# Performance work log

Hardware: AMD Instinct MI355X
Metric: run time of the kernel (lower is better)

Reference implementation:

```python
import jax, jax.numpy as jnp
import numpy as np

N, F, E = 1024, 32, 20


def setup_inputs() -> dict:
    key = jax.random.key(0)
    ks = jax.random.split(key, 18)
    f32 = jnp.float32
    nrm = lambda k, shape, s=1.0: (jax.random.normal(k, shape, f32) * s)
    scalar = nrm(ks[0], (N, 1, F))
    vector = nrm(ks[1], (N, 3, F))
    expansion = nrm(ks[2], (N, N, E))
    d = nrm(ks[3], (N, N, 3))
    direction = d / (jnp.linalg.norm(d, axis=-1, keepdims=True) + 1e-6)
    mask = (jax.random.uniform(ks[4], (N, N, 1)) < 0.9).astype(f32)
    w = 0.1  # weight scale
    return {
        "scalar": scalar, "vector": vector, "expansion": expansion,
        "direction": direction, "mask": mask,
        # message.msg_left: Linear(F,F) -> SiLU -> Linear(F,3F)
        "mL_w1": nrm(ks[5], (F, F), w), "mL_b1": jnp.zeros((F,), f32),
        "mL_w2": nrm(ks[6], (F, 3 * F), w), "mL_b2": jnp.zeros((3 * F,), f32),
        # message.msg_right: Linear(E, 3F)
        "mR_w": nrm(ks[7], (E, 3 * F), w), "mR_b": jnp.zeros((3 * F,), f32),
        # update.upd_right: Linear(2F,F) -> SiLU -> Linear(F,3F)
        "uR_w1": nrm(ks[8], (2 * F, F), w), "uR_b1": jnp.zeros((F,), f32),
        "uR_w2": nrm(ks[9], (F, 3 * F), w), "uR_b2": jnp.zeros((3 * F,), f32),
        # update.U / update.V: Linear(F,F,bias=False)
        "U_w": nrm(ks[10], (F, F), w),
        "V_w": nrm(ks[11], (F, F), w),
    }


def _message(s, v, expansion, direction, mask,
             mL_w1, mL_b1, mL_w2, mL_b2, mR_w, mR_b):
    # msg_left(s): [N,1,F] -> [N,1,3F]
    left = jax.nn.silu(s @ mL_w1 + mL_b1) @ mL_w2 + mL_b2
    # msg_right(expansion): [N,N,E] -> [N,N,3F] -> [N,N,1,3F]
    right = (expansion @ mR_w + mR_b)[..., None, :]
    prod = left * right                      # [N,N,1,3F]
    a, b, c = jnp.split(prod, 3, axis=-1)    # each [N,N,1,F]
    mask_ = mask[..., None]                  # [N,N,1,1]
    delta_s = jnp.sum(mask_ * b, axis=-3)    # [N,1,F]
    dv = v * a + direction[..., None] * c    # [N,N,3,F]
    delta_v = jnp.sum(mask_ * dv, axis=-3)   # [N,3,F]
    return delta_s, delta_v


def _update(scalar, vector, uR_w1, uR_b1, uR_w2, uR_b2, U_w, V_w):
    left = vector @ U_w                      # [N,3,F]
    right = vector @ V_w                     # [N,3,F]
    right_norm = jnp.linalg.norm(right, axis=-2, keepdims=True)   # [N,1,F]
    feats = jnp.concatenate((scalar, right_norm), axis=-1)        # [N,1,2F]
    feats = jax.nn.silu(feats @ uR_w1 + uR_b1) @ uR_w2 + uR_b2    # [N,1,3F]
    a, b, c = jnp.split(feats, 3, axis=-1)
    delta_v = a * left                                            # [N,3,F]
    inner = jnp.sum(left * right, axis=-2, keepdims=True)         # [N,1,F]
    delta_s = inner * b + c
    return delta_s, delta_v


def reference(scalar, vector, expansion, direction, mask,
              mL_w1, mL_b1, mL_w2, mL_b2, mR_w, mR_b,
              uR_w1, uR_b1, uR_w2, uR_b2, U_w, V_w):
    ds, dv = _message(scalar, vector, expansion, direction, mask,
                      mL_w1, mL_b1, mL_w2, mL_b2, mR_w, mR_b)
    scalar = scalar + ds
    vector = vector + dv
    ds, dv = _update(scalar, vector, uR_w1, uR_b1, uR_w2, uR_b2, U_w, V_w)
    return scalar + ds, vector + dv
```

## Files before the change

### kernel.cpp

```cpp
#include <hip/hip_runtime.h>
#include <hip/hip_bf16.h>
#include <math.h>

#define NN 1024
#define KJ 32
#define NCHUNK (NN / KJ)
#define LP 40

typedef __attribute__((ext_vector_type(8))) short v8s;
typedef __attribute__((ext_vector_type(4))) float v4f;

#define MFMA(a, b, c) __builtin_amdgcn_mfma_f32_16x16x32_bf16((a), (b), (c), 0, 0, 0)

static __device__ __forceinline__ float silu_f(float x) {
    return x / (1.0f + __expf(-x));
}
static __device__ __forceinline__ unsigned short f2bf(float x) {
    __hip_bfloat16 h = __float2bfloat16(x);
    unsigned short u; __builtin_memcpy(&u, &h, 2); return u;
}
static __device__ __forceinline__ unsigned pack2bf(float lo, float hi) {
    __hip_bfloat162 h = __float22bfloat162_rn(make_float2(lo, hi));
    unsigned u; __builtin_memcpy(&u, &h, 4); return u;
}

extern "C" __global__ __launch_bounds__(128)
void node_kernel(const float* __restrict__ scalar,
                 const float* __restrict__ vector,
                 const float* __restrict__ mL_w1, const float* __restrict__ mL_b1,
                 const float* __restrict__ mL_w2, const float* __restrict__ mL_b2,
                 unsigned short* __restrict__ RT)
{
    const int j = blockIdx.x;
    const int t = threadIdx.x;
    __shared__ float ss[32], sh[32], sleft[96];

    if (t < 32) ss[t] = scalar[j * 32 + t];
    __syncthreads();
    if (t < 32) {
        float a = mL_b1[t];
        #pragma unroll
        for (int k = 0; k < 32; k++) a = fmaf(ss[k], mL_w1[k * 32 + t], a);
        sh[t] = silu_f(a);
    }
    __syncthreads();
    if (t < 96) {
        float a = mL_b2[t];
        #pragma unroll
        for (int k = 0; k < 32; k++) a = fmaf(sh[k], mL_w2[k * 96 + t], a);
        sleft[t] = a;
    }
    __syncthreads();
    for (int n = t; n < 160; n += 128) {
        float val;
        if (n < 32)        val = sleft[32 + n];
        else if (n < 128)  val = vector[j * 96 + (n - 32)] * sleft[(n - 32) & 31];
        else               val = sleft[64 + (n - 128)];
        RT[(size_t)n * NN + j] = f2bf(val);
    }
}

extern "C" __global__ __launch_bounds__(128, 3)
void edge_mfma_kernel(const float* __restrict__ scalar,
                      const float* __restrict__ vector,
                      const float* __restrict__ expansion,
                      const float* __restrict__ direction,
                      const float* __restrict__ mask,
                      const float* __restrict__ mR_w, const float* __restrict__ mR_b,
                      const float* __restrict__ uR_w1, const float* __restrict__ uR_b1,
                      const float* __restrict__ uR_w2, const float* __restrict__ uR_b2,
                      const float* __restrict__ U_w,  const float* __restrict__ V_w,
                      const unsigned short* __restrict__ RT,
                      float* __restrict__ out)
{
    const int i = blockIdx.x;
    const int t = threadIdx.x;
    const int wave = t >> 6;
    const int lane = t & 63;
    const int lrow = lane & 15;
    const int quad = lane >> 4;
    const int jp = lane >> 2;
    const int g  = lane & 3;
    const int jl = jp * 2;

    __shared__ __align__(16) char smem[18944];
    unsigned short* L1 = (unsigned short*)smem;
    unsigned short* L2 = (unsigned short*)(smem + 2560);
    float* T1c = (float*)smem;
    float* T2c = (float*)(smem + 10752);
    __shared__ float snew[32], vnew[96], lUs[96], rVs[96], rnorm[32], h2s[32], f2s[96];

    v4f acc[16];
    #pragma unroll
    for (int q = 0; q < 16; ++q) acc[q] = (v4f){0.f, 0.f, 0.f, 0.f};

    if (wave == 0) {
        for (int ch = 0; ch < NCHUNK; ++ch) {
            const int j0 = ch * KJ;
            const size_t jg = (size_t)i * NN + j0 + jl;
            const float4 fa = *(const float4*)(expansion + jg * 20 + 4 * g);
            const float4 fb = *(const float4*)(expansion + (jg + 1) * 20 + 4 * g);
            const float m0 = mask[jg], m1 = mask[jg + 1];
            {
                const float ea[4] = {fa.x, fa.y, fa.z, fa.w};
                const float eb[4] = {fb.x, fb.y, fb.z, fb.w};
                #pragma unroll
                for (int k = 0; k < 4; ++k)
                    *(unsigned*)(L1 + (4 * g + k) * LP + jl) = pack2bf(m0 * ea[k], m1 * eb[k]);
            }
            if (g == 3) {
                const float4 ca = *(const float4*)(expansion + jg * 20 + 16);
                const float4 cb = *(const float4*)(expansion + (jg + 1) * 20 + 16);
                const float ea[4] = {ca.x, ca.y, ca.z, ca.w};
                const float eb[4] = {cb.x, cb.y, cb.z, cb.w};
                #pragma unroll
                for (int k = 0; k < 4; ++k)
                    *(unsigned*)(L1 + (16 + k) * LP + jl) = pack2bf(m0 * ea[k], m1 * eb[k]);
            }
            if (g == 0) *(unsigned*)(L1 + 20 * LP + jl) = pack2bf(m0, m1);

            const int koff = quad * 8;
            const v8s a0 = *(const v8s*)(L1 + lrow * LP + koff);
            const v8s a1 = *(const v8s*)(L1 + (16 + lrow) * LP + koff);
            const unsigned short* Bp = RT + (size_t)lrow * NN + j0 + koff;
            #pragma unroll
            for (int nt = 0; nt < 8; ++nt) {
                const v8s b = *(const v8s*)(Bp + (size_t)nt * 16 * NN);
                acc[nt]     = MFMA(a0, b, acc[nt]);
                acc[8 + nt] = MFMA(a1, b, acc[8 + nt]);
            }
        }
    } else {
        for (int ch = 0; ch < NCHUNK; ++ch) {
            const int j0 = ch * KJ;
            const size_t jg = (size_t)i * NN + j0 + jl;
            const float m0 = mask[jg], m1 = mask[jg + 1];
            const float pa[3] = {m0 * direction[jg * 3 + 0],
                                 m0 * direction[jg * 3 + 1],
                                 m0 * direction[jg * 3 + 2]};
            const float pb[3] = {m1 * direction[(jg + 1) * 3 + 0],
                                 m1 * direction[(jg + 1) * 3 + 1],
                                 m1 * direction[(jg + 1) * 3 + 2]};
            const float4 fa = *(const float4*)(expansion + jg * 20 + 4 * g);
            const float4 fb = *(const float4*)(expansion + (jg + 1) * 20 + 4 * g);
            const float ea[4] = {fa.x, fa.y, fa.z, fa.w};
            const float eb[4] = {fb.x, fb.y, fb.z, fb.w};
            #pragma unroll
            for (int d = 0; d < 3; ++d)
                #pragma unroll
                for (int k = 0; k < 4; ++k)
                    *(unsigned*)(L2 + (d * 20 + 4 * g + k) * LP + jl) =
                        pack2bf(pa[d] * ea[k], pb[d] * eb[k]);
            if (g < 3) {
                const float4 ca = *(const float4*)(expansion + jg * 20 + 16);
                const float4 cb = *(const float4*)(expansion + (jg + 1) * 20 + 16);
                const float sa = (g == 0) ? pa[0] : ((g == 1) ? pa[1] : pa[2]);
                const float sb = (g == 0) ? pb[0] : ((g == 1) ? pb[1] : pb[2]);
                const float ea4[4] = {ca.x, ca.y, ca.z, ca.w};
                const float eb4[4] = {cb.x, cb.y, cb.z, cb.w};
                #pragma unroll
                for (int k = 0; k < 4; ++k)
                    *(unsigned*)(L2 + (g * 20 + 16 + k) * LP + jl) =
                        pack2bf(sa * ea4[k], sb * eb4[k]);
            } else {
                #pragma unroll
                for (int d = 0; d < 3; ++d)
                    *(unsigned*)(L2 + (60 + d) * LP + jl) = pack2bf(pa[d], pb[d]);
            }

            const int koff = quad * 8;
            const v8s c0 = *(const v8s*)(L2 + (lrow) * LP + koff);
            const v8s c1 = *(const v8s*)(L2 + (16 + lrow) * LP + koff);
            const v8s c2 = *(const v8s*)(L2 + (32 + lrow) * LP + koff);
            const v8s c3 = *(const v8s*)(L2 + (48 + lrow) * LP + koff);
            const unsigned short* Bp = RT + (size_t)(128 + lrow) * NN + j0 + koff;
            const v8s b0 = *(const v8s*)(Bp);
            const v8s b1 = *(const v8s*)(Bp + (size_t)16 * NN);
            acc[0] = MFMA(c0, b0, acc[0]); acc[1] = MFMA(c0, b1, acc[1]);
            acc[2] = MFMA(c1, b0, acc[2]); acc[3] = MFMA(c1, b1, acc[3]);
            acc[4] = MFMA(c2, b0, acc[4]); acc[5] = MFMA(c2, b1, acc[5]);
            acc[6] = MFMA(c3, b0, acc[6]); acc[7] = MFMA(c3, b1, acc[7]);
        }
    }

    __syncthreads();
    if (wave == 0) {
        #pragma unroll
        for (int mt = 0; mt < 2; ++mt)
        #pragma unroll
        for (int nt = 0; nt < 8; ++nt)
        #pragma unroll
        for (int r = 0; r < 4; ++r) {
            const int row = mt * 16 + quad * 4 + r;
            if (row <= 20) T1c[row * 128 + nt * 16 + lrow] = acc[mt * 8 + nt][r];
        }
    } else {
        #pragma unroll
        for (int mt = 0; mt < 4; ++mt)
        #pragma unroll
        for (int nb = 0; nb < 2; ++nb)
        #pragma unroll
        for (int r = 0; r < 4; ++r) {
            const int row = mt * 16 + quad * 4 + r;
            if (row <= 62) T2c[row * 32 + nb * 16 + lrow] = acc[mt * 2 + nb][r];
        }
    }
    __syncthreads();

    if (t < 32) {
        const int f = t;
        float a = mR_b[32 + f] * T1c[20 * 128 + f];
        #pragma unroll
        for (int e = 0; e < 20; ++e) a = fmaf(mR_w[e * 96 + 32 + f], T1c[e * 128 + f], a);
        snew[f] = scalar[i * 32 + f] + a;
    } else if (t < 128) {
        const int q = t - 32, d = q >> 5, f = q & 31;
        const int col = 32 + q;
        float a = mR_b[f] * T1c[20 * 128 + col];
        #pragma unroll
        for (int e = 0; e < 20; ++e) a = fmaf(mR_w[e * 96 + f], T1c[e * 128 + col], a);
        float c = mR_b[64 + f] * T2c[(60 + d) * 32 + f];
        #pragma unroll
        for (int e = 0; e < 20; ++e) c = fmaf(mR_w[e * 96 + 64 + f], T2c[(d * 20 + e) * 32 + f], c);
        vnew[q] = vector[i * 96 + q] + a + c;
    }
    __syncthreads();

    if (t < 96) {
        const int d = t >> 5, f = t & 31;
        float au = 0.f, av = 0.f;
        #pragma unroll
        for (int k = 0; k < 32; ++k) {
            const float vv = vnew[d * 32 + k];
            au = fmaf(vv, U_w[k * 32 + f], au);
            av = fmaf(vv, V_w[k * 32 + f], av);
        }
        lUs[t] = au; rVs[t] = av;
    }
    __syncthreads();
    if (t < 32)
        rnorm[t] = sqrtf(rVs[t] * rVs[t] + rVs[32 + t] * rVs[32 + t] + rVs[64 + t] * rVs[64 + t]);
    __syncthreads();
    if (t < 32) {
        float a = uR_b1[t];
        #pragma unroll
        for (int k = 0; k < 32; ++k) a = fmaf(snew[k], uR_w1[k * 32 + t], a);
        #pragma unroll
        for (int k = 0; k < 32; ++k) a = fmaf(rnorm[k], uR_w1[(32 + k) * 32 + t], a);
        h2s[t] = silu_f(a);
    }
    __syncthreads();
    if (t < 96) {
        float a = uR_b2[t];
        #pragma unroll
        for (int k = 0; k < 32; ++k) a = fmaf(h2s[k], uR_w2[k * 96 + t], a);
        f2s[t] = a;
    }
    __syncthreads();
    if (t < 32) {
        const float inner = lUs[t] * rVs[t] + lUs[32 + t] * rVs[32 + t] + lUs[64 + t] * rVs[64 + t];
        out[i * 32 + t] = snew[t] + inner * f2s[32 + t] + f2s[64 + t];
    }
    if (t < 96) {
        out[32768 + i * 96 + t] = vnew[t] + f2s[t & 31] * lUs[t];
    }
}

extern "C" void kernel_launch(void* const* d_in, const int* in_sizes, int n_in,
                              void* d_out, int out_size, void* d_ws, size_t ws_size,
                              hipStream_t stream) {
    const float* scalar    = (const float*)d_in[0];
    const float* vector    = (const float*)d_in[1];
    const float* expansion = (const float*)d_in[2];
    const float* direction = (const float*)d_in[3];
    const float* mask      = (const float*)d_in[4];
    const float* mL_w1     = (const float*)d_in[5];
    const float* mL_b1     = (const float*)d_in[6];
    const float* mL_w2     = (const float*)d_in[7];
    const float* mL_b2     = (const float*)d_in[8];
    const float* mR_w      = (const float*)d_in[9];
    const float* mR_b      = (const float*)d_in[10];
    const float* uR_w1     = (const float*)d_in[11];
    const float* uR_b1     = (const float*)d_in[12];
    const float* uR_w2     = (const float*)d_in[13];
    const float* uR_b2     = (const float*)d_in[14];
    const float* U_w       = (const float*)d_in[15];
    const float* V_w       = (const float*)d_in[16];
    float* out = (float*)d_out;
    unsigned short* RT = (unsigned short*)d_ws;

    hipLaunchKernelGGL(node_kernel, dim3(NN), dim3(128), 0, stream,
                       scalar, vector, mL_w1, mL_b1, mL_w2, mL_b2, RT);
    hipLaunchKernelGGL(edge_mfma_kernel, dim3(NN), dim3(128), 0, stream,
                       scalar, vector, expansion, direction, mask,
                       mR_w, mR_b, uR_w1, uR_b1, uR_w2, uR_b2, U_w, V_w,
                       RT, out);
}
```

Baseline: 229.8 us.

## Split edge reduction across four waves and prefetch next chunk's inputs

The edge kernel now runs 256 threads, so each of the two roles (expansion path and direction path) is handled by two waves. Each wave reduces half of the j-chunks, and the partial accumulators are summed through shared memory in an extra synchronized pass. Each wave also loads the next chunk's expansion, mask and direction values into registers before processing the current chunk, hiding global-load latency. This raises parallelism and memory-level concurrency per block, at the cost of more register pressure, an added reduction step and more LDS staging. Threads 128-255 are idle during the epilogue.

```diff
diff --git a/kernel.cpp b/kernel.cpp
--- a/kernel.cpp
+++ b/kernel.cpp
@@ -5,6 +5,7 @@
 #define NN 1024
 #define KJ 32
 #define NCHUNK (NN / KJ)
+#define HCH (NCHUNK / 2)
 #define LP 40
 
 typedef __attribute__((ext_vector_type(8))) short v8s;
@@ -60,7 +61,7 @@
     }
 }
 
-extern "C" __global__ __launch_bounds__(128, 3)
+extern "C" __global__ __launch_bounds__(256, 4)
 void edge_mfma_kernel(const float* __restrict__ scalar,
                       const float* __restrict__ vector,
                       const float* __restrict__ expansion,
@@ -82,10 +83,11 @@
     const int jp = lane >> 2;
     const int g  = lane & 3;
     const int jl = jp * 2;
+    const int half = wave & 1;
 
     __shared__ __align__(16) char smem[18944];
-    unsigned short* L1 = (unsigned short*)smem;
-    unsigned short* L2 = (unsigned short*)(smem + 2560);
+    unsigned short* L1 = (unsigned short*)smem + half * (32 * LP);
+    unsigned short* L2 = (unsigned short*)(smem + 5120) + half * (64 * LP);
     float* T1c = (float*)smem;
     float* T2c = (float*)(smem + 10752);
     __shared__ float snew[32], vnew[96], lUs[96], rVs[96], rnorm[32], h2s[32], f2s[96];
@@ -94,13 +96,34 @@
     #pragma unroll
     for (int q = 0; q < 16; ++q) acc[q] = (v4f){0.f, 0.f, 0.f, 0.f};
 
-    if (wave == 0) {
-        for (int ch = 0; ch < NCHUNK; ++ch) {
-            const int j0 = ch * KJ;
-            const size_t jg = (size_t)i * NN + j0 + jl;
-            const float4 fa = *(const float4*)(expansion + jg * 20 + 4 * g);
-            const float4 fb = *(const float4*)(expansion + (jg + 1) * 20 + 4 * g);
-            const float m0 = mask[jg], m1 = mask[jg + 1];
+    const int ch0 = half * HCH;
+    const int chEnd = ch0 + HCH;
+
+    if (wave < 2) {
+        float4 fa, fb, ca, cb; float m0, m1;
+        {
+            const size_t jg = (size_t)i * NN + ch0 * KJ + jl;
+            fa = *(const float4*)(expansion + jg * 20 + 4 * g);
+            fb = *(const float4*)(expansion + (jg + 1) * 20 + 4 * g);
+            m0 = mask[jg]; m1 = mask[jg + 1];
+            if (g == 3) {
+                ca = *(const float4*)(expansion + jg * 20 + 16);
+                cb = *(const float4*)(expansion + (jg + 1) * 20 + 16);
+            } else { ca = fa; cb = fb; }
+        }
+        for (int ch = ch0; ch < chEnd; ++ch) {
+            float4 nfa, nfb, nca, ncb; float nm0, nm1;
+            {
+                const int pch = (ch + 1 < chEnd) ? (ch + 1) : ch;
+                const size_t jg = (size_t)i * NN + pch * KJ + jl;
+                nfa = *(const float4*)(expansion + jg * 20 + 4 * g);
+                nfb = *(const float4*)(expansion + (jg + 1) * 20 + 4 * g);
+                nm0 = mask[jg]; nm1 = mask[jg + 1];
+                if (g == 3) {
+                    nca = *(const float4*)(expansion + jg * 20 + 16);
+                    ncb = *(const float4*)(expansion + (jg + 1) * 20 + 16);
+                } else { nca = nfa; ncb = nfb; }
+            }
             {
                 const float ea[4] = {fa.x, fa.y, fa.z, fa.w};
                 const float eb[4] = {fb.x, fb.y, fb.z, fb.w};
@@ -109,8 +132,6 @@
                     *(unsigned*)(L1 + (4 * g + k) * LP + jl) = pack2bf(m0 * ea[k], m1 * eb[k]);
             }
             if (g == 3) {
-                const float4 ca = *(const float4*)(expansion + jg * 20 + 16);
-                const float4 cb = *(const float4*)(expansion + (jg + 1) * 20 + 16);
                 const float ea[4] = {ca.x, ca.y, ca.z, ca.w};
                 const float eb[4] = {cb.x, cb.y, cb.z, cb.w};
                 #pragma unroll
@@ -119,6 +140,7 @@
             }
             if (g == 0) *(unsigned*)(L1 + 20 * LP + jl) = pack2bf(m0, m1);
 
+            const int j0 = ch * KJ;
             const int koff = quad * 8;
             const v8s a0 = *(const v8s*)(L1 + lrow * LP + koff);
             const v8s a1 = *(const v8s*)(L1 + (16 + lrow) * LP + koff);
@@ -129,45 +151,64 @@
                 acc[nt]     = MFMA(a0, b, acc[nt]);
                 acc[8 + nt] = MFMA(a1, b, acc[8 + nt]);
             }
+            fa = nfa; fb = nfb; ca = nca; cb = ncb; m0 = nm0; m1 = nm1;
         }
     } else {
-        for (int ch = 0; ch < NCHUNK; ++ch) {
-            const int j0 = ch * KJ;
-            const size_t jg = (size_t)i * NN + j0 + jl;
-            const float m0 = mask[jg], m1 = mask[jg + 1];
-            const float pa[3] = {m0 * direction[jg * 3 + 0],
-                                 m0 * direction[jg * 3 + 1],
-                                 m0 * direction[jg * 3 + 2]};
-            const float pb[3] = {m1 * direction[(jg + 1) * 3 + 0],
-                                 m1 * direction[(jg + 1) * 3 + 1],
-                                 m1 * direction[(jg + 1) * 3 + 2]};
-            const float4 fa = *(const float4*)(expansion + jg * 20 + 4 * g);
-            const float4 fb = *(const float4*)(expansion + (jg + 1) * 20 + 4 * g);
-            const float ea[4] = {fa.x, fa.y, fa.z, fa.w};
-            const float eb[4] = {fb.x, fb.y, fb.z, fb.w};
-            #pragma unroll
-            for (int d = 0; d < 3; ++d)
-                #pragma unroll
-                for (int k = 0; k < 4; ++k)
-                    *(unsigned*)(L2 + (d * 20 + 4 * g + k) * LP + jl) =
-                        pack2bf(pa[d] * ea[k], pb[d] * eb[k]);
+        float4 fa, fb, ca, cb; float m0, m1, da0, da1, da2, db0, db1, db2;
+        {
+            const size_t jg = (size_t)i * NN + ch0 * KJ + jl;
+            fa = *(const float4*)(expansion + jg * 20 + 4 * g);
+            fb = *(const float4*)(expansion + (jg + 1) * 20 + 4 * g);
+            m0 = mask[jg]; m1 = mask[jg + 1];
+            da0 = direction[jg * 3 + 0]; da1 = direction[jg * 3 + 1]; da2 = direction[jg * 3 + 2];
+            db0 = direction[(jg + 1) * 3 + 0]; db1 = direction[(jg + 1) * 3 + 1]; db2 = direction[(jg + 1) * 3 + 2];
             if (g < 3) {
-                const float4 ca = *(const float4*)(expansion + jg * 20 + 16);
-                const float4 cb = *(const float4*)(expansion + (jg + 1) * 20 + 16);
-                const float sa = (g == 0) ? pa[0] : ((g == 1) ? pa[1] : pa[2]);
-                const float sb = (g == 0) ? pb[0] : ((g == 1) ? pb[1] : pb[2]);
-                const float ea4[4] = {ca.x, ca.y, ca.z, ca.w};
-                const float eb4[4] = {cb.x, cb.y, cb.z, cb.w};
-                #pragma unroll
-                for (int k = 0; k < 4; ++k)
-                    *(unsigned*)(L2 + (g * 20 + 16 + k) * LP + jl) =
-                        pack2bf(sa * ea4[k], sb * eb4[k]);
-            } else {
+                ca = *(const float4*)(expansion + jg * 20 + 16);
+                cb = *(const float4*)(expansion + (jg + 1) * 20 + 16);
+            } else { ca = fa; cb = fb; }
+        }
+        for (int ch = ch0; ch < chEnd; ++ch) {
+            float4 nfa, nfb, nca, ncb; float nm0, nm1, nda0, nda1, nda2, ndb0, ndb1, ndb2;
+            {
+                const int pch = (ch + 1 < chEnd) ? (ch + 1) : ch;
+                const size_t jg = (size_t)i * NN + pch * KJ + jl;
+                nfa = *(const float4*)(expansion + jg * 20 + 4 * g);
+                nfb = *(const float4*)(expansion + (jg + 1) * 20 + 4 * g);
+                nm0 = mask[jg]; nm1 = mask[jg + 1];
+                nda0 = direction[jg * 3 + 0]; nda1 = direction[jg * 3 + 1]; nda2 = direction[jg * 3 + 2];
+                ndb0 = direction[(jg + 1) * 3 + 0]; ndb1 = direction[(jg + 1) * 3 + 1]; ndb2 = direction[(jg + 1) * 3 + 2];
+                if (g < 3) {
+                    nca = *(const float4*)(expansion + jg * 20 + 16);
+                    ncb = *(const float4*)(expansion + (jg + 1) * 20 + 16);
+                } else { nca = nfa; ncb = nfb; }
+            }
+            {
+                const float pa[3] = {m0 * da0, m0 * da1, m0 * da2};
+                const float pb[3] = {m1 * db0, m1 * db1, m1 * db2};
+                const float ea[4] = {fa.x, fa.y, fa.z, fa.w};
+                const float eb[4] = {fb.x, fb.y, fb.z, fb.w};
                 #pragma unroll
                 for (int d = 0; d < 3; ++d)
-                    *(unsigned*)(L2 + (60 + d) * LP + jl) = pack2bf(pa[d], pb[d]);
-            }
-
+                    #pragma unroll
+                    for (int k = 0; k < 4; ++k)
+                        *(unsigned*)(L2 + (d * 20 + 4 * g + k) * LP + jl) =
+                            pack2bf(pa[d] * ea[k], pb[d] * eb[k]);
+                if (g < 3) {
+                    const float sa = (g == 0) ? pa[0] : ((g == 1) ? pa[1] : pa[2]);
+                    const float sb = (g == 0) ? pb[0] : ((g == 1) ? pb[1] : pb[2]);
+                    const float ea4[4] = {ca.x, ca.y, ca.z, ca.w};
+                    const float eb4[4] = {cb.x, cb.y, cb.z, cb.w};
+                    #pragma unroll
+                    for (int k = 0; k < 4; ++k)
+                        *(unsigned*)(L2 + (g * 20 + 16 + k) * LP + jl) =
+                            pack2bf(sa * ea4[k], sb * eb4[k]);
+                } else {
+                    #pragma unroll
+                    for (int d = 0; d < 3; ++d)
+                        *(unsigned*)(L2 + (60 + d) * LP + jl) = pack2bf(pa[d], pb[d]);
+                }
+            }
+            const int j0 = ch * KJ;
             const int koff = quad * 8;
             const v8s c0 = *(const v8s*)(L2 + (lrow) * LP + koff);
             const v8s c1 = *(const v8s*)(L2 + (16 + lrow) * LP + koff);
@@ -180,6 +221,8 @@
             acc[2] = MFMA(c1, b0, acc[2]); acc[3] = MFMA(c1, b1, acc[3]);
             acc[4] = MFMA(c2, b0, acc[4]); acc[5] = MFMA(c2, b1, acc[5]);
             acc[6] = MFMA(c3, b0, acc[6]); acc[7] = MFMA(c3, b1, acc[7]);
+            fa = nfa; fb = nfb; ca = nca; cb = ncb; m0 = nm0; m1 = nm1;
+            da0 = nda0; da1 = nda1; da2 = nda2; db0 = ndb0; db1 = ndb1; db2 = ndb2;
         }
     }
 
@@ -194,7 +237,7 @@
             const int row = mt * 16 + quad * 4 + r;
             if (row <= 20) T1c[row * 128 + nt * 16 + lrow] = acc[mt * 8 + nt][r];
         }
-    } else {
+    } else if (wave == 2) {
         #pragma unroll
         for (int mt = 0; mt < 4; ++mt)
         #pragma unroll
@@ -203,6 +246,28 @@
         for (int r = 0; r < 4; ++r) {
             const int row = mt * 16 + quad * 4 + r;
             if (row <= 62) T2c[row * 32 + nb * 16 + lrow] = acc[mt * 2 + nb][r];
+        }
+    }
+    __syncthreads();
+    if (wave == 1) {
+        #pragma unroll
+        for (int mt = 0; mt < 2; ++mt)
+        #pragma unroll
+        for (int nt = 0; nt < 8; ++nt)
+        #pragma unroll
+        for (int r = 0; r < 4; ++r) {
+            const int row = mt * 16 + quad * 4 + r;
+            if (row <= 20) T1c[row * 128 + nt * 16 + lrow] += acc[mt * 8 + nt][r];
+        }
+    } else if (wave == 3) {
+        #pragma unroll
+        for (int mt = 0; mt < 4; ++mt)
+        #pragma unroll
+        for (int nb = 0; nb < 2; ++nb)
+        #pragma unroll
+        for (int r = 0; r < 4; ++r) {
+            const int row = mt * 16 + quad * 4 + r;
+            if (row <= 62) T2c[row * 32 + nb * 16 + lrow] += acc[mt * 2 + nb][r];
         }
     }
     __syncthreads();
@@ -291,7 +356,7 @@
 
     hipLaunchKernelGGL(node_kernel, dim3(NN), dim3(128), 0, stream,
                        scalar, vector, mL_w1, mL_b1, mL_w2, mL_b2, RT);
-    hipLaunchKernelGGL(edge_mfma_kernel, dim3(NN), dim3(128), 0, stream,
+    hipLaunchKernelGGL(edge_mfma_kernel, dim3(NN), dim3(256), 0, stream,
                        scalar, vector, expansion, direction, mask,
                        mR_w, mR_b, uR_w1, uR_b1, uR_w2, uR_b2, U_w, V_w,
                        RT, out);
```

Measured after the change: 216.0 us. 1.06x faster.

## Split edge reduction over j-slices with LDS-staged RT and atomic partials

Applied to the files above, without the earlier changes.

Restructures the edge kernel so each block handles 8 nodes by a 64-wide j slice. The slice of the RT matrix is staged once in LDS and reused by all four waves, each covering two i rows, instead of every block streaming RT from global memory. Expansion, mask and direction loads are prefetched one step ahead. Partial results are reduced into a zeroed workspace via atomicAdd, and the node-update tail moves to a separate combine kernel. This adds a memset, a third launch and atomic traffic in exchange for better reuse and more parallel work.

```diff
diff --git a/kernel.cpp b/kernel.cpp
--- a/kernel.cpp
+++ b/kernel.cpp
@@ -3,9 +3,10 @@
 #include <math.h>
 
 #define NN 1024
-#define KJ 32
-#define NCHUNK (NN / KJ)
+#define JS 64
+#define PB 72
 #define LP 40
+#define LROWS 85
 
 typedef __attribute__((ext_vector_type(8))) short v8s;
 typedef __attribute__((ext_vector_type(4))) float v4f;
@@ -60,20 +61,14 @@
     }
 }
 
-extern "C" __global__ __launch_bounds__(128, 3)
-void edge_mfma_kernel(const float* __restrict__ scalar,
-                      const float* __restrict__ vector,
-                      const float* __restrict__ expansion,
+extern "C" __global__ __launch_bounds__(256, 3)
+void edge_mfma_kernel(const float* __restrict__ expansion,
                       const float* __restrict__ direction,
                       const float* __restrict__ mask,
                       const float* __restrict__ mR_w, const float* __restrict__ mR_b,
-                      const float* __restrict__ uR_w1, const float* __restrict__ uR_b1,
-                      const float* __restrict__ uR_w2, const float* __restrict__ uR_b2,
-                      const float* __restrict__ U_w,  const float* __restrict__ V_w,
                       const unsigned short* __restrict__ RT,
-                      float* __restrict__ out)
+                      float* __restrict__ part)
 {
-    const int i = blockIdx.x;
     const int t = threadIdx.x;
     const int wave = t >> 6;
     const int lane = t & 63;
@@ -83,186 +78,228 @@
     const int g  = lane & 3;
     const int jl = jp * 2;
 
-    __shared__ __align__(16) char smem[18944];
-    unsigned short* L1 = (unsigned short*)smem;
-    unsigned short* L2 = (unsigned short*)(smem + 2560);
-    float* T1c = (float*)smem;
-    float* T2c = (float*)(smem + 10752);
-    __shared__ float snew[32], vnew[96], lUs[96], rVs[96], rnorm[32], h2s[32], f2s[96];
-
-    v4f acc[16];
+    const int bx = blockIdx.x;
+    const int slice = bx & 15;
+    const int i0 = (bx >> 4) * 8;
+    const int j0s = slice * JS;
+
+    __shared__ __align__(16) unsigned short BSm[160 * PB];
+    __shared__ __align__(16) unsigned short Lm[4 * LROWS * LP];
+
+    for (int u = t; u < 160 * 8; u += 256) {
+        const int row = u >> 3, seg = u & 7;
+        *(uint4*)(BSm + row * PB + seg * 8) =
+            *(const uint4*)(RT + (size_t)row * NN + j0s + seg * 8);
+    }
+    __syncthreads();
+
+    unsigned short* L1 = Lm + wave * (LROWS * LP);
+    unsigned short* L2 = L1 + 21 * LP;
+    float* S = (float*)L1;
+
+    v4f acc[24];
     #pragma unroll
-    for (int q = 0; q < 16; ++q) acc[q] = (v4f){0.f, 0.f, 0.f, 0.f};
-
-    if (wave == 0) {
-        for (int ch = 0; ch < NCHUNK; ++ch) {
-            const int j0 = ch * KJ;
-            const size_t jg = (size_t)i * NN + j0 + jl;
-            const float4 fa = *(const float4*)(expansion + jg * 20 + 4 * g);
-            const float4 fb = *(const float4*)(expansion + (jg + 1) * 20 + 4 * g);
-            const float m0 = mask[jg], m1 = mask[jg + 1];
+    for (int q = 0; q < 24; ++q) acc[q] = (v4f){0.f, 0.f, 0.f, 0.f};
+
+    const int iw = i0 + wave * 2;
+
+    float4 fa, fb, ca, cb;
+    float m0, m1, da0, da1, da2, db0, db1, db2;
+    {
+        const size_t jg = (size_t)iw * NN + j0s + jl;
+        fa = *(const float4*)(expansion + jg * 20 + 4 * g);
+        fb = *(const float4*)(expansion + (jg + 1) * 20 + 4 * g);
+        ca = *(const float4*)(expansion + jg * 20 + 16);
+        cb = *(const float4*)(expansion + (jg + 1) * 20 + 16);
+        m0 = mask[jg]; m1 = mask[jg + 1];
+        da0 = direction[jg * 3 + 0]; da1 = direction[jg * 3 + 1]; da2 = direction[jg * 3 + 2];
+        db0 = direction[(jg + 1) * 3 + 0]; db1 = direction[(jg + 1) * 3 + 1]; db2 = direction[(jg + 1) * 3 + 2];
+    }
+
+    for (int it = 0; it < 2; ++it) {
+        const int i = iw + it;
+        for (int ch = 0; ch < 2; ++ch) {
             {
+                const float pa0 = m0 * da0, pa1 = m0 * da1, pa2 = m0 * da2;
+                const float pb0 = m1 * db0, pb1 = m1 * db1, pb2 = m1 * db2;
                 const float ea[4] = {fa.x, fa.y, fa.z, fa.w};
                 const float eb[4] = {fb.x, fb.y, fb.z, fb.w};
+                const float caa[4] = {ca.x, ca.y, ca.z, ca.w};
+                const float cbb[4] = {cb.x, cb.y, cb.z, cb.w};
                 #pragma unroll
                 for (int k = 0; k < 4; ++k)
                     *(unsigned*)(L1 + (4 * g + k) * LP + jl) = pack2bf(m0 * ea[k], m1 * eb[k]);
-            }
-            if (g == 3) {
-                const float4 ca = *(const float4*)(expansion + jg * 20 + 16);
-                const float4 cb = *(const float4*)(expansion + (jg + 1) * 20 + 16);
-                const float ea[4] = {ca.x, ca.y, ca.z, ca.w};
-                const float eb[4] = {cb.x, cb.y, cb.z, cb.w};
-                #pragma unroll
-                for (int k = 0; k < 4; ++k)
-                    *(unsigned*)(L1 + (16 + k) * LP + jl) = pack2bf(m0 * ea[k], m1 * eb[k]);
-            }
-            if (g == 0) *(unsigned*)(L1 + 20 * LP + jl) = pack2bf(m0, m1);
-
-            const int koff = quad * 8;
-            const v8s a0 = *(const v8s*)(L1 + lrow * LP + koff);
-            const v8s a1 = *(const v8s*)(L1 + (16 + lrow) * LP + koff);
-            const unsigned short* Bp = RT + (size_t)lrow * NN + j0 + koff;
-            #pragma unroll
-            for (int nt = 0; nt < 8; ++nt) {
-                const v8s b = *(const v8s*)(Bp + (size_t)nt * 16 * NN);
-                acc[nt]     = MFMA(a0, b, acc[nt]);
-                acc[8 + nt] = MFMA(a1, b, acc[8 + nt]);
-            }
-        }
-    } else {
-        for (int ch = 0; ch < NCHUNK; ++ch) {
-            const int j0 = ch * KJ;
-            const size_t jg = (size_t)i * NN + j0 + jl;
-            const float m0 = mask[jg], m1 = mask[jg + 1];
-            const float pa[3] = {m0 * direction[jg * 3 + 0],
-                                 m0 * direction[jg * 3 + 1],
-                                 m0 * direction[jg * 3 + 2]};
-            const float pb[3] = {m1 * direction[(jg + 1) * 3 + 0],
-                                 m1 * direction[(jg + 1) * 3 + 1],
-                                 m1 * direction[(jg + 1) * 3 + 2]};
-            const float4 fa = *(const float4*)(expansion + jg * 20 + 4 * g);
-            const float4 fb = *(const float4*)(expansion + (jg + 1) * 20 + 4 * g);
-            const float ea[4] = {fa.x, fa.y, fa.z, fa.w};
-            const float eb[4] = {fb.x, fb.y, fb.z, fb.w};
-            #pragma unroll
-            for (int d = 0; d < 3; ++d)
-                #pragma unroll
-                for (int k = 0; k < 4; ++k)
-                    *(unsigned*)(L2 + (d * 20 + 4 * g + k) * LP + jl) =
-                        pack2bf(pa[d] * ea[k], pb[d] * eb[k]);
-            if (g < 3) {
-                const float4 ca = *(const float4*)(expansion + jg * 20 + 16);
-                const float4 cb = *(const float4*)(expansion + (jg + 1) * 20 + 16);
-                const float sa = (g == 0) ? pa[0] : ((g == 1) ? pa[1] : pa[2]);
-                const float sb = (g == 0) ? pb[0] : ((g == 1) ? pb[1] : pb[2]);
-                const float ea4[4] = {ca.x, ca.y, ca.z, ca.w};
-                const float eb4[4] = {cb.x, cb.y, cb.z, cb.w};
-                #pragma unroll
-                for (int k = 0; k < 4; ++k)
-                    *(unsigned*)(L2 + (g * 20 + 16 + k) * LP + jl) =
-                        pack2bf(sa * ea4[k], sb * eb4[k]);
-            } else {
+                if (g == 3) {
+                    #pragma unroll
+                    for (int k = 0; k < 4; ++k)
+                        *(unsigned*)(L1 + (16 + k) * LP + jl) = pack2bf(m0 * caa[k], m1 * cbb[k]);
+                }
+                if (g == 0) *(unsigned*)(L1 + 20 * LP + jl) = pack2bf(m0, m1);
+
+                const float pad[3] = {pa0, pa1, pa2};
+                const float pbd[3] = {pb0, pb1, pb2};
                 #pragma unroll
                 for (int d = 0; d < 3; ++d)
-                    *(unsigned*)(L2 + (60 + d) * LP + jl) = pack2bf(pa[d], pb[d]);
-            }
-
-            const int koff = quad * 8;
-            const v8s c0 = *(const v8s*)(L2 + (lrow) * LP + koff);
-            const v8s c1 = *(const v8s*)(L2 + (16 + lrow) * LP + koff);
-            const v8s c2 = *(const v8s*)(L2 + (32 + lrow) * LP + koff);
-            const v8s c3 = *(const v8s*)(L2 + (48 + lrow) * LP + koff);
-            const unsigned short* Bp = RT + (size_t)(128 + lrow) * NN + j0 + koff;
-            const v8s b0 = *(const v8s*)(Bp);
-            const v8s b1 = *(const v8s*)(Bp + (size_t)16 * NN);
-            acc[0] = MFMA(c0, b0, acc[0]); acc[1] = MFMA(c0, b1, acc[1]);
-            acc[2] = MFMA(c1, b0, acc[2]); acc[3] = MFMA(c1, b1, acc[3]);
-            acc[4] = MFMA(c2, b0, acc[4]); acc[5] = MFMA(c2, b1, acc[5]);
-            acc[6] = MFMA(c3, b0, acc[6]); acc[7] = MFMA(c3, b1, acc[7]);
+                    #pragma unroll
+                    for (int k = 0; k < 4; ++k)
+                        *(unsigned*)(L2 + (d * 20 + 4 * g + k) * LP + jl) =
+                            pack2bf(pad[d] * ea[k], pbd[d] * eb[k]);
+                if (g < 3) {
+                    const float sa = (g == 0) ? pa0 : ((g == 1) ? pa1 : pa2);
+                    const float sb = (g == 0) ? pb0 : ((g == 1) ? pb1 : pb2);
+                    #pragma unroll
+                    for (int k = 0; k < 4; ++k)
+                        *(unsigned*)(L2 + (g * 20 + 16 + k) * LP + jl) =
+                            pack2bf(sa * caa[k], sb * cbb[k]);
+                } else {
+                    *(unsigned*)(L2 + (60 + 0) * LP + jl) = pack2bf(pa0, pb0);
+                    *(unsigned*)(L2 + (60 + 1) * LP + jl) = pack2bf(pa1, pb1);
+                    *(unsigned*)(L2 + (60 + 2) * LP + jl) = pack2bf(pa2, pb2);
+                }
+            }
+            {
+                const int u = it * 2 + ch;
+                const int un = (u < 3) ? u + 1 : 3;
+                const int itn = un >> 1, chn = un & 1;
+                const size_t jg = (size_t)(iw + itn) * NN + j0s + chn * 32 + jl;
+                fa = *(const float4*)(expansion + jg * 20 + 4 * g);
+                fb = *(const float4*)(expansion + (jg + 1) * 20 + 4 * g);
+                ca = *(const float4*)(expansion + jg * 20 + 16);
+                cb = *(const float4*)(expansion + (jg + 1) * 20 + 16);
+                m0 = mask[jg]; m1 = mask[jg + 1];
+                da0 = direction[jg * 3 + 0]; da1 = direction[jg * 3 + 1]; da2 = direction[jg * 3 + 2];
+                db0 = direction[(jg + 1) * 3 + 0]; db1 = direction[(jg + 1) * 3 + 1]; db2 = direction[(jg + 1) * 3 + 2];
+            }
+            {
+                const int ko = quad * 8;
+                const int kl = ch * 32 + ko;
+                const v8s a0 = *(const v8s*)(L1 + lrow * LP + ko);
+                const v8s a1 = *(const v8s*)(L1 + (16 + lrow) * LP + ko);
+                #pragma unroll
+                for (int nt = 0; nt < 8; ++nt) {
+                    const v8s b = *(const v8s*)(BSm + (nt * 16 + lrow) * PB + kl);
+                    acc[nt]     = MFMA(a0, b, acc[nt]);
+                    acc[8 + nt] = MFMA(a1, b, acc[8 + nt]);
+                }
+                const v8s c0 = *(const v8s*)(L2 + (lrow) * LP + ko);
+                const v8s c1 = *(const v8s*)(L2 + (16 + lrow) * LP + ko);
+                const v8s c2 = *(const v8s*)(L2 + (32 + lrow) * LP + ko);
+                const v8s c3 = *(const v8s*)(L2 + (48 + lrow) * LP + ko);
+                const v8s b0 = *(const v8s*)(BSm + (128 + lrow) * PB + kl);
+                const v8s b1 = *(const v8s*)(BSm + (144 + lrow) * PB + kl);
+                acc[16] = MFMA(c0, b0, acc[16]); acc[17] = MFMA(c0, b1, acc[17]);
+                acc[18] = MFMA(c1, b0, acc[18]); acc[19] = MFMA(c1, b1, acc[19]);
+                acc[20] = MFMA(c2, b0, acc[20]); acc[21] = MFMA(c2, b1, acc[21]);
+                acc[22] = MFMA(c3, b0, acc[22]); acc[23] = MFMA(c3, b1, acc[23]);
+            }
         }
-    }
-
-    __syncthreads();
-    if (wave == 0) {
-        #pragma unroll
-        for (int mt = 0; mt < 2; ++mt)
-        #pragma unroll
-        for (int nt = 0; nt < 8; ++nt)
-        #pragma unroll
-        for (int r = 0; r < 4; ++r) {
-            const int row = mt * 16 + quad * 4 + r;
-            if (row <= 20) T1c[row * 128 + nt * 16 + lrow] = acc[mt * 8 + nt][r];
+
+        #pragma unroll
+        for (int h = 0; h < 2; ++h) {
+            #pragma unroll
+            for (int mt = 0; mt < 2; ++mt)
+            #pragma unroll
+            for (int q = 0; q < 4; ++q)
+            #pragma unroll
+            for (int r = 0; r < 4; ++r) {
+                const int row = mt * 16 + quad * 4 + r;
+                if (row <= 20) S[row * 64 + q * 16 + lrow] = acc[mt * 8 + h * 4 + q][r];
+            }
+            const int col = h * 64 + lane;
+            const int fw = (col < 32) ? (32 + col) : ((col - 32) & 31);
+            float v = mR_b[fw] * S[20 * 64 + lane];
+            #pragma unroll
+            for (int e = 0; e < 20; ++e) v = fmaf(mR_w[e * 96 + fw], S[e * 64 + lane], v);
+            atomicAdd(part + (size_t)i * 224 + col, v);
         }
-    } else {
-        #pragma unroll
-        for (int mt = 0; mt < 4; ++mt)
-        #pragma unroll
-        for (int nb = 0; nb < 2; ++nb)
-        #pragma unroll
-        for (int r = 0; r < 4; ++r) {
-            const int row = mt * 16 + quad * 4 + r;
-            if (row <= 62) T2c[row * 32 + nb * 16 + lrow] = acc[mt * 2 + nb][r];
+        #pragma unroll
+        for (int h2 = 0; h2 < 2; ++h2) {
+            #pragma unroll
+            for (int mt = 0; mt < 4; ++mt)
+            #pragma unroll
+            for (int r = 0; r < 4; ++r) {
+                const int row = mt * 16 + quad * 4 + r;
+                if (row <= 62) S[row * 16 + lrow] = acc[16 + mt * 2 + h2][r];
+            }
+            if (lane < 48) {
+                const int dd = lane >> 4, f16 = lane & 15;
+                const int f = h2 * 16 + f16;
+                float v = mR_b[64 + f] * S[(60 + dd) * 16 + f16];
+                #pragma unroll
+                for (int e = 0; e < 20; ++e)
+                    v = fmaf(mR_w[e * 96 + 64 + f], S[(dd * 20 + e) * 16 + f16], v);
+                atomicAdd(part + (size_t)i * 224 + 128 + dd * 32 + f, v);
+            }
         }
-    }
-    __syncthreads();
-
+        #pragma unroll
+        for (int q = 0; q < 24; ++q) acc[q] = (v4f){0.f, 0.f, 0.f, 0.f};
+    }
+}
+
+extern "C" __global__ __launch_bounds__(256)
+void combine_kernel(const float* __restrict__ scalar,
+                    const float* __restrict__ vector,
+                    const float* __restrict__ uR_w1, const float* __restrict__ uR_b1,
+                    const float* __restrict__ uR_w2, const float* __restrict__ uR_b2,
+                    const float* __restrict__ U_w,  const float* __restrict__ V_w,
+                    const float* __restrict__ part,
+                    float* __restrict__ out)
+{
+    const int i = blockIdx.x;
+    const int t = threadIdx.x;
+    __shared__ float snew[32], vnew[96];
+    __shared__ float lU[96], rV[96], rnorm[32], h2[32], f2[96];
+
+    if (t < 128) {
+        float a = part[(size_t)i * 224 + t];
+        if (t >= 32) a += part[(size_t)i * 224 + 96 + t];
+        const int d = t >> 5, ff = t & 31;
+        if (d == 0) snew[ff] = scalar[i * 32 + ff] + a;
+        else        vnew[(d - 1) * 32 + ff] = vector[i * 96 + (d - 1) * 32 + ff] + a;
+    }
+    __syncthreads();
+
+    if (t < 96) {
+        const int d = t >> 5, ff = t & 31;
+        float a = 0.0f;
+        #pragma unroll
+        for (int k = 0; k < 32; k++) a = fmaf(vnew[d * 32 + k], U_w[k * 32 + ff], a);
+        lU[t] = a;
+    } else if (t >= 128 && t < 224) {
+        const int dt = t - 128, d = dt >> 5, ff = dt & 31;
+        float a = 0.0f;
+        #pragma unroll
+        for (int k = 0; k < 32; k++) a = fmaf(vnew[d * 32 + k], V_w[k * 32 + ff], a);
+        rV[dt] = a;
+    }
+    __syncthreads();
     if (t < 32) {
-        const int f = t;
-        float a = mR_b[32 + f] * T1c[20 * 128 + f];
-        #pragma unroll
-        for (int e = 0; e < 20; ++e) a = fmaf(mR_w[e * 96 + 32 + f], T1c[e * 128 + f], a);
-        snew[f] = scalar[i * 32 + f] + a;
-    } else if (t < 128) {
-        const int q = t - 32, d = q >> 5, f = q & 31;
-        const int col = 32 + q;
-        float a = mR_b[f] * T1c[20 * 128 + col];
-        #pragma unroll
-        for (int e = 0; e < 20; ++e) a = fmaf(mR_w[e * 96 + f], T1c[e * 128 + col], a);
-        float c = mR_b[64 + f] * T2c[(60 + d) * 32 + f];
-        #pragma unroll
-        for (int e = 0; e < 20; ++e) c = fmaf(mR_w[e * 96 + 64 + f], T2c[(d * 20 + e) * 32 + f], c);
-        vnew[q] = vector[i * 96 + q] + a + c;
-    }
-    __syncthreads();
-
-    if (t < 96) {
-        const int d = t >> 5, f = t & 31;
-        float au = 0.f, av = 0.f;
-        #pragma unroll
-        for (int k = 0; k < 32; ++k) {
-            const float vv = vnew[d * 32 + k];
-            au = fmaf(vv, U_w[k * 32 + f], au);
-            av = fmaf(vv, V_w[k * 32 + f], av);
-        }
-        lUs[t] = au; rVs[t] = av;
-    }
-    __syncthreads();
-    if (t < 32)
-        rnorm[t] = sqrtf(rVs[t] * rVs[t] + rVs[32 + t] * rVs[32 + t] + rVs[64 + t] * rVs[64 + t]);
+        const float a = rV[t] * rV[t] + rV[32 + t] * rV[32 + t] + rV[64 + t] * rV[64 + t];
+        rnorm[t] = sqrtf(a);
+    }
     __syncthreads();
     if (t < 32) {
         float a = uR_b1[t];
         #pragma unroll
-        for (int k = 0; k < 32; ++k) a = fmaf(snew[k], uR_w1[k * 32 + t], a);
-        #pragma unroll
-        for (int k = 0; k < 32; ++k) a = fmaf(rnorm[k], uR_w1[(32 + k) * 32 + t], a);
-        h2s[t] = silu_f(a);
+        for (int k = 0; k < 32; k++) a = fmaf(snew[k],  uR_w1[k * 32 + t], a);
+        #pragma unroll
+        for (int k = 0; k < 32; k++) a = fmaf(rnorm[k], uR_w1[(32 + k) * 32 + t], a);
+        h2[t] = silu_f(a);
     }
     __syncthreads();
     if (t < 96) {
         float a = uR_b2[t];
         #pragma unroll
-        for (int k = 0; k < 32; ++k) a = fmaf(h2s[k], uR_w2[k * 96 + t], a);
-        f2s[t] = a;
+        for (int k = 0; k < 32; k++) a = fmaf(h2[k], uR_w2[k * 96 + t], a);
+        f2[t] = a;
     }
     __syncthreads();
     if (t < 32) {
-        const float inner = lUs[t] * rVs[t] + lUs[32 + t] * rVs[32 + t] + lUs[64 + t] * rVs[64 + t];
-        out[i * 32 + t] = snew[t] + inner * f2s[32 + t] + f2s[64 + t];
-    }
-    if (t < 96) {
-        out[32768 + i * 96 + t] = vnew[t] + f2s[t & 31] * lUs[t];
+        const float inner = lU[t] * rV[t] + lU[32 + t] * rV[32 + t] + lU[64 + t] * rV[64 + t];
+        out[i * 32 + t] = snew[t] + inner * f2[32 + t] + f2[64 + t];
+    } else if (t >= 64 && t < 160) {
+        const int dt = t - 64, ff = dt & 31;
+        out[32768 + i * 96 + dt] = vnew[dt] + f2[ff] * lU[dt];
     }
 }
 
@@ -287,12 +324,16 @@
     const float* U_w       = (const float*)d_in[15];
     const float* V_w       = (const float*)d_in[16];
     float* out = (float*)d_out;
+
     unsigned short* RT = (unsigned short*)d_ws;
+    float* part = (float*)((char*)d_ws + 160 * NN * 2);
 
     hipLaunchKernelGGL(node_kernel, dim3(NN), dim3(128), 0, stream,
                        scalar, vector, mL_w1, mL_b1, mL_w2, mL_b2, RT);
-    hipLaunchKernelGGL(edge_mfma_kernel, dim3(NN), dim3(128), 0, stream,
-                       scalar, vector, expansion, direction, mask,
-                       mR_w, mR_b, uR_w1, uR_b1, uR_w2, uR_b2, U_w, V_w,
-                       RT, out);
-}
+    hipMemsetAsync(part, 0, (size_t)NN * 224 * sizeof(float), stream);
+    hipLaunchKernelGGL(edge_mfma_kernel, dim3(2048), dim3(256), 0, stream,
+                       expansion, direction, mask, mR_w, mR_b, RT, part);
+    hipLaunchKernelGGL(combine_kernel, dim3(NN), dim3(256), 0, stream,
+                       scalar, vector, uR_w1, uR_b1, uR_w2, uR_b2, U_w, V_w,
+                       part, out);
+}
```

Measured after the change: 443.4 us. 1.93x slower.
